# Optimization experiments

Hardware: AMD Instinct MI355X
Metric: run time of the kernel (lower is better)

The kernel has to match this reference:

```python
import jax, jax.numpy as jnp
import numpy as np

N_NODES = 10000
N_EDGES = 320000
IN_DIM = 256
HID = 64
HEADS = 4
OUT_DIM = 64
NEG_SLOPE = 0.2


def setup_inputs() -> dict:
    key = jax.random.key(0)
    ks = jax.random.split(key, 10)
    s = 0.05
    return {
        "h": jax.random.normal(ks[0], (N_NODES, IN_DIM), jnp.float32),
        "src": jax.random.randint(ks[1], (N_EDGES,), 0, N_NODES, jnp.int32),
        "dst": jax.random.randint(ks[2], (N_EDGES,), 0, N_NODES, jnp.int32),
        "W1": jax.random.normal(ks[3], (IN_DIM, HEADS * HID), jnp.float32) * s,
        "al1": jax.random.normal(ks[4], (HEADS, HID), jnp.float32) * s,
        "ar1": jax.random.normal(ks[5], (HEADS, HID), jnp.float32) * s,
        "b1": jnp.zeros((HEADS * HID,), jnp.float32),
        "W2": jax.random.normal(ks[6], (HEADS * HID, OUT_DIM), jnp.float32) * s,
        "al2": jax.random.normal(ks[7], (1, OUT_DIM), jnp.float32) * s,
        "ar2": jax.random.normal(ks[8], (1, OUT_DIM), jnp.float32) * s,
        "b2": jnp.zeros((OUT_DIM,), jnp.float32),
    }


def _gatconv(h, W, al, ar, b, src, dst, n_heads, d_out):
    """DGL-style GATConv: project, edge-softmax attention, scatter-aggregate."""
    n = h.shape[0]
    feat = (h @ W).reshape(n, n_heads, d_out)          # [N,H,D]
    el = jnp.sum(feat * al, axis=-1)                   # [N,H]
    er = jnp.sum(feat * ar, axis=-1)                   # [N,H]
    e = jax.nn.leaky_relu(el[src] + er[dst], NEG_SLOPE)  # [E,H]
    # segment softmax over incoming edges of each dst node
    m = jax.ops.segment_max(e, dst, num_segments=n)    # [N,H]
    ex = jnp.exp(e - m[dst])                           # [E,H]
    denom = jax.ops.segment_sum(ex, dst, num_segments=n)  # [N,H]
    alpha = ex / denom[dst]                            # [E,H]
    msg = feat[src] * alpha[:, :, None]                # [E,H,D]
    out = jax.ops.segment_sum(msg, dst, num_segments=n)  # [N,H,D]
    return out + b.reshape(n_heads, d_out)


def reference(h, src, dst, W1, al1, ar1, b1, W2, al2, ar2, b2):
    h1 = _gatconv(h, W1, al1, ar1, b1, src, dst, HEADS, HID)
    h1 = jax.nn.elu(h1.reshape(N_NODES, HEADS * HID))  # flatten(1) then ELU
    h2 = _gatconv(h1, W2, al2, ar2, b2, src, dst, 1, OUT_DIM)
    return jnp.squeeze(h2, axis=1)  # [N, OUT_DIM]
```

## Files before the change

### kernel.cpp

```cpp
#include <hip/hip_runtime.h>
#include <hip/hip_bf16.h>
#include <stdint.h>

#define NN 10000
#define NE 320000
#define NH 4
#define BCAP 128

#define GEMM1_MB 79
#define GEMM1_BLOCKS (GEMM1_MB * 4)
#define BUILD_BLOCKS 1250

typedef __attribute__((ext_vector_type(8))) short s16x8;
typedef __attribute__((ext_vector_type(4))) float f32x4;
typedef __attribute__((ext_vector_type(8))) unsigned short u16x8;

static __device__ __forceinline__ float b2f(unsigned short u) {
    union { unsigned int i; float f; } x; x.i = ((unsigned int)u) << 16; return x.f;
}
static __device__ __forceinline__ unsigned short f2b(float f) {
    unsigned int u = __float_as_uint(f);
    unsigned int r = (u + 0x7fffu + ((u >> 16) & 1u)) >> 16;
    return (unsigned short)r;
}

__global__ __launch_bounds__(256) void k_prep(const unsigned short* __restrict__ hraw,
                        const void* __restrict__ W1, const void* __restrict__ W2,
                        const void* al1, const void* ar1, const void* b1,
                        const void* al2, const void* ar2, const void* b2,
                        unsigned short* __restrict__ W1T, unsigned short* __restrict__ W2T,
                        unsigned short* __restrict__ canon, int* __restrict__ cnt,
                        int* __restrict__ flag) {
    __shared__ int sb[256];
    int t = threadIdx.x;
    int c = 0;
    for (int i = t; i < 2048; i += 256) {
        unsigned short u = hraw[i];
        int e = (u >> 7) & 0xFF;
        c += (e >= 97 && e <= 157) ? 1 : 0;
    }
    sb[t] = c;
    __syncthreads();
    for (int o = 128; o > 0; o >>= 1) {
        if (t < o) sb[t] += sb[t + o];
        __syncthreads();
    }
    int isbf = (sb[0] >= 1741) ? 1 : 0;

    int idx = blockIdx.x * 256 + t;
    if (idx < 65536) {
        int n = idx >> 8, k = idx & 255;
        W1T[idx] = isbf ? ((const unsigned short*)W1)[k * 256 + n]
                        : f2b(((const float*)W1)[k * 256 + n]);
    } else if (idx < 81920) {
        int j = idx - 65536;
        int n = j >> 8, k = j & 255;
        W2T[j] = isbf ? ((const unsigned short*)W2)[k * 64 + n]
                      : f2b(((const float*)W2)[k * 64 + n]);
    } else if (idx < 82880) {
        int j = idx - 81920;
        const void* srcp; int q;
        if      (j < 256) { srcp = al1; q = j; }
        else if (j < 512) { srcp = ar1; q = j - 256; }
        else if (j < 768) { srcp = b1;  q = j - 512; }
        else if (j < 832) { srcp = al2; q = j - 768; }
        else if (j < 896) { srcp = ar2; q = j - 832; }
        else              { srcp = b2;  q = j - 896; }
        canon[j] = isbf ? ((const unsigned short*)srcp)[q] : f2b(((const float*)srcp)[q]);
    } else if (idx < 92880) {
        cnt[idx - 82880] = 0;
    } else if (idx == 92880) {
        flag[0] = isbf;
    }
}

#define BSTRIDE 264
static __device__ __forceinline__ void gemm_body(short* Bs,
                        const void* __restrict__ A, const unsigned short* __restrict__ BT,
                        unsigned short* __restrict__ C,
                        float* __restrict__ el, float* __restrict__ er,
                        const unsigned short* __restrict__ al,
                        const unsigned short* __restrict__ ar,
                        int M, int N, int H, int a_isbf, int mtile, int head) {
    int t = threadIdx.x;
    int wave = t >> 6, lane = t & 63;
    int m0 = mtile * 128;
    const unsigned short* Bh = BT + (size_t)head * 64 * 256;

#pragma unroll
    for (int i = 0; i < 8; ++i) {
        int idx = t + i * 256;
        int row = idx >> 5, chunk = idx & 31;
        *(s16x8*)&Bs[row * BSTRIDE + chunk * 8] =
            *(const s16x8*)&Bh[(size_t)row * 256 + chunk * 8];
    }
    __syncthreads();

    int kq = (lane >> 4) * 8;
    const unsigned short* Ab = (const unsigned short*)A;
    const float*          Af = (const float*)A;
    int aR[2];
#pragma unroll
    for (int mi = 0; mi < 2; ++mi) {
        int aRow = m0 + mi * 64 + wave * 16 + (lane & 15);
        aR[mi] = (aRow < M) ? aRow : M - 1;
    }
    f32x4 acc[2][4] = {};

#pragma unroll
    for (int k0 = 0; k0 < 256; k0 += 32) {
        s16x8 afr[2];
#pragma unroll
        for (int mi = 0; mi < 2; ++mi) {
            if (a_isbf) {
                afr[mi] = *(const s16x8*)&Ab[(size_t)aR[mi] * 256 + k0 + kq];
            } else {
                const float* pf = &Af[(size_t)aR[mi] * 256 + k0 + kq];
                float4 x0 = *(const float4*)pf;
                float4 x1 = *(const float4*)(pf + 4);
                afr[mi][0] = (short)f2b(x0.x); afr[mi][1] = (short)f2b(x0.y);
                afr[mi][2] = (short)f2b(x0.z); afr[mi][3] = (short)f2b(x0.w);
                afr[mi][4] = (short)f2b(x1.x); afr[mi][5] = (short)f2b(x1.y);
                afr[mi][6] = (short)f2b(x1.z); afr[mi][7] = (short)f2b(x1.w);
            }
        }
#pragma unroll
        for (int nt = 0; nt < 4; ++nt) {
            s16x8 bfr = *(const s16x8*)&Bs[(nt * 16 + (lane & 15)) * BSTRIDE + k0 + kq];
            acc[0][nt] = __builtin_amdgcn_mfma_f32_16x16x32_bf16(afr[0], bfr, acc[0][nt], 0, 0, 0);
            acc[1][nt] = __builtin_amdgcn_mfma_f32_16x16x32_bf16(afr[1], bfr, acc[1][nt], 0, 0, 0);
        }
    }

    float alv[4], arv[4];
#pragma unroll
    for (int nt = 0; nt < 4; ++nt) {
        int c = (lane & 15) + nt * 16;
        alv[nt] = b2f(al[head * 64 + c]);
        arv[nt] = b2f(ar[head * 64 + c]);
    }
    int col0 = head * 64 + (lane & 15);
#pragma unroll
    for (int mi = 0; mi < 2; ++mi) {
        int r0 = m0 + mi * 64 + wave * 16 + (lane >> 4) * 4;
        float cr[4][4];
#pragma unroll
        for (int nt = 0; nt < 4; ++nt) {
            int col = col0 + nt * 16;
#pragma unroll
            for (int i = 0; i < 4; ++i) {
                unsigned short cb = f2b(acc[mi][nt][i]);
                cr[nt][i] = b2f(cb);
                int r = r0 + i;
                if (r < M) C[(size_t)r * N + col] = cb;
            }
        }
#pragma unroll
        for (int i = 0; i < 4; ++i) {
            float pl = 0.f, pr = 0.f;
#pragma unroll
            for (int nt = 0; nt < 4; ++nt) {
                pl += cr[nt][i] * alv[nt];
                pr += cr[nt][i] * arv[nt];
            }
#pragma unroll
            for (int o = 1; o < 16; o <<= 1) {
                pl += __shfl_xor(pl, o, 64);
                pr += __shfl_xor(pr, o, 64);
            }
            int r = r0 + i;
            if ((lane & 15) == 0 && r < M) {
                el[(size_t)r * H + head] = pl;
                er[(size_t)r * H + head] = pr;
            }
        }
    }
}

__global__ __launch_bounds__(256) void k_g1b(const void* __restrict__ A,
                        const unsigned short* __restrict__ W1T,
                        unsigned short* __restrict__ feat1,
                        float* __restrict__ el, float* __restrict__ er,
                        const unsigned short* __restrict__ al,
                        const unsigned short* __restrict__ ar,
                        const int* __restrict__ flagp,
                        const int* __restrict__ src, const int* __restrict__ dst,
                        int* __restrict__ cnt, int* __restrict__ bucket) {
    __shared__ short Bs[64 * BSTRIDE];
    int bid = blockIdx.x;
    if (bid < GEMM1_BLOCKS) {
        int head = bid / GEMM1_MB;
        int mtile = bid - head * GEMM1_MB;
        gemm_body(Bs, A, W1T, feat1, el, er, al, ar, NN, 256, NH, flagp[0], mtile, head);
    } else {
        int i = (bid - GEMM1_BLOCKS) * 256 + threadIdx.x;
        if (i < NE) {
            int d = dst[i];
            int pos = atomicAdd(&cnt[d], 1);
            if (pos < BCAP) bucket[(d << 7) + pos] = src[i];
        }
    }
}

__global__ __launch_bounds__(256) void k_gemm(const void* __restrict__ A,
                                              const unsigned short* __restrict__ BT,
                                              unsigned short* __restrict__ C,
                                              float* __restrict__ el, float* __restrict__ er,
                                              const unsigned short* __restrict__ al,
                                              const unsigned short* __restrict__ ar,
                                              int M, int N, int H) {
    __shared__ short Bs[64 * BSTRIDE];
    gemm_body(Bs, A, BT, C, el, er, al, ar, M, N, H, 1, blockIdx.x, blockIdx.y);
}

__global__ __launch_bounds__(256) void k_edge1(const int* __restrict__ cnt,
                        const int* __restrict__ bucket,
                        const float* __restrict__ el, const float* __restrict__ er,
                        const unsigned short* __restrict__ feat,
                        const unsigned short* __restrict__ b1,
                        unsigned short* __restrict__ h1) {
    __shared__ int   s_s[128];
    __shared__ float s_w[128][4];
    int node = blockIdx.x;
    int t = threadIdx.x;
    int head = t >> 6, lane = t & 63;
    int eg = lane >> 3, d8 = lane & 7;
    int end = cnt[node]; if (end > BCAP) end = BCAP;
    const int* bkt = bucket + ((size_t)node << 7);
    float4 er4 = *(const float4*)&er[(size_t)node * 4];
    float lsum = 0.f;
    float a[8] = {};
    for (int cbase = 0; cbase < end; cbase += 128) {
        int cn = end - cbase; if (cn > 128) cn = 128;
        __syncthreads();
        if (t < cn) {
            int s = bkt[cbase + t];
            s_s[t] = s;
            float4 el4 = *(const float4*)&el[(size_t)s * 4];
            float x0 = el4.x + er4.x; x0 = (x0 >= 0.f) ? x0 : 0.2f * x0;
            float x1 = el4.y + er4.y; x1 = (x1 >= 0.f) ? x1 : 0.2f * x1;
            float x2 = el4.z + er4.z; x2 = (x2 >= 0.f) ? x2 : 0.2f * x2;
            float x3 = el4.w + er4.w; x3 = (x3 >= 0.f) ? x3 : 0.2f * x3;
            s_w[t][0] = __expf(x0);
            s_w[t][1] = __expf(x1);
            s_w[t][2] = __expf(x2);
            s_w[t][3] = __expf(x3);
        } else if (t < ((cn + 7) & ~7)) {
            s_s[t] = 0;
            s_w[t][0] = 0.f; s_w[t][1] = 0.f; s_w[t][2] = 0.f; s_w[t][3] = 0.f;
        }
        __syncthreads();
        int niter = (cn + 7) >> 3;
#pragma unroll 2
        for (int i = 0; i < niter; ++i) {
            int idx = 8 * i + eg;
            float we = s_w[idx][head];
            int   se = s_s[idx];
            if (d8 == 0) lsum += we;
            u16x8 fv = *(const u16x8*)&feat[(((size_t)se * NH + head) << 6) + (d8 << 3)];
#pragma unroll
            for (int j = 0; j < 8; ++j) a[j] += we * b2f(fv[j]);
        }
    }
#pragma unroll
    for (int o = 1; o < 64; o <<= 1) lsum += __shfl_xor(lsum, o, 64);
#pragma unroll
    for (int j = 0; j < 8; ++j) {
        a[j] += __shfl_xor(a[j], 8, 64);
        a[j] += __shfl_xor(a[j], 16, 64);
        a[j] += __shfl_xor(a[j], 32, 64);
    }
    if (eg == 0) {
        float inv = (lsum > 0.f) ? 1.f / lsum : 0.f;
        u16x8 r;
#pragma unroll
        for (int j = 0; j < 8; ++j) {
            float o = a[j] * inv + b2f(b1[head * 64 + d8 * 8 + j]);
            o = (o > 0.f) ? o : (__expf(o) - 1.f);
            r[j] = f2b(o);
        }
        *(u16x8*)&h1[(((size_t)node * NH + head) << 6) + d8 * 8] = r;
    }
}

__global__ __launch_bounds__(256) void k_edge2(const int* __restrict__ cnt,
                        const int* __restrict__ bucket,
                        const float* __restrict__ el, const float* __restrict__ er,
                        const unsigned short* __restrict__ feat,
                        const unsigned short* __restrict__ b2,
                        void* __restrict__ out, const int* __restrict__ flagp) {
    int wave = threadIdx.x >> 6, lane = threadIdx.x & 63;
    int node = blockIdx.x * 4 + wave;
    if (node >= NN) return;
    int eg = lane >> 3, d8 = lane & 7;
    int isbf = flagp[0];
    int end = cnt[node]; if (end > BCAP) end = BCAP;
    const int* bkt = bucket + ((size_t)node << 7);
    float er_d = er[node];
    float lsum = 0.f;
    float a[8] = {};
    for (int base = 0; base < end; base += 64) {
        int c = base + lane;
        float wgt = 0.f; int s = 0;
        if (c < end) {
            s = bkt[c];
            float x = el[s] + er_d;
            x = (x >= 0.f) ? x : 0.2f * x;
            wgt = __expf(x);
        }
        lsum += wgt;
        int cn = end - base; if (cn > 64) cn = 64;
        int niter = (cn + 7) >> 3;
#pragma unroll 2
        for (int i = 0; i < niter; ++i) {
            int idx = 8 * i + eg;
            float we = __shfl(wgt, idx, 64);
            int   se = __shfl(s, idx, 64);
            u16x8 fv = *(const u16x8*)&feat[((size_t)se << 6) + (d8 << 3)];
#pragma unroll
            for (int j = 0; j < 8; ++j) a[j] += we * b2f(fv[j]);
        }
    }
#pragma unroll
    for (int o = 1; o < 64; o <<= 1) lsum += __shfl_xor(lsum, o, 64);
#pragma unroll
    for (int j = 0; j < 8; ++j) {
        a[j] += __shfl_xor(a[j], 8, 64);
        a[j] += __shfl_xor(a[j], 16, 64);
        a[j] += __shfl_xor(a[j], 32, 64);
    }
    if (eg == 0) {
        float inv = (lsum > 0.f) ? 1.f / lsum : 0.f;
        float o[8];
#pragma unroll
        for (int j = 0; j < 8; ++j) o[j] = a[j] * inv + b2f(b2[d8 * 8 + j]);
        size_t ob = ((size_t)node << 6) + d8 * 8;
        if (isbf) {
            u16x8 r;
#pragma unroll
            for (int j = 0; j < 8; ++j) r[j] = f2b(o[j]);
            *(u16x8*)&((unsigned short*)out)[ob] = r;
        } else {
            float4 r0, r1;
            r0.x = o[0]; r0.y = o[1]; r0.z = o[2]; r0.w = o[3];
            r1.x = o[4]; r1.y = o[5]; r1.z = o[6]; r1.w = o[7];
            *(float4*)&((float*)out)[ob] = r0;
            *(float4*)&((float*)out)[ob + 4] = r1;
        }
    }
}

extern "C" void kernel_launch(void* const* d_in, const int* in_sizes, int n_in,
                              void* d_out, int out_size, void* d_ws, size_t ws_size,
                              hipStream_t stream) {
    const void* h   = d_in[0];
    const int*  src = (const int*)d_in[1];
    const int*  dst = (const int*)d_in[2];
    const void* W1  = d_in[3];
    const void* al1 = d_in[4];
    const void* ar1 = d_in[5];
    const void* b1  = d_in[6];
    const void* W2  = d_in[7];
    const void* al2 = d_in[8];
    const void* ar2 = d_in[9];
    const void* b2  = d_in[10];

    char* w = (char*)d_ws;
    size_t off = 0;
    auto alloc = [&](size_t bytes) -> void* {
        void* p = w + off;
        off = (off + bytes + 255) & ~(size_t)255;
        return p;
    };
    int* flag               = (int*)alloc(8);
    int* cnt                = (int*)alloc(NN * 4);
    int* bucket             = (int*)alloc((size_t)NN * BCAP * 4);
    unsigned short* canon   = (unsigned short*)alloc(960 * 2);
    unsigned short* W1T     = (unsigned short*)alloc(256 * 256 * 2);
    unsigned short* W2T     = (unsigned short*)alloc(64 * 256 * 2);
    unsigned short* feat1   = (unsigned short*)alloc((size_t)NN * 256 * 2);
    float* el1              = (float*)alloc(NN * NH * 4);
    float* er1              = (float*)alloc(NN * NH * 4);
    unsigned short* h1      = (unsigned short*)alloc((size_t)NN * 256 * 2);
    unsigned short* feat2   = (unsigned short*)alloc((size_t)NN * 64 * 2);
    float* el2              = (float*)alloc(NN * 4);
    float* er2              = (float*)alloc(NN * 4);
    (void)ws_size; (void)in_sizes; (void)n_in; (void)out_size;

    unsigned short* cal1 = canon + 0;
    unsigned short* car1 = canon + 256;
    unsigned short* cb1  = canon + 512;
    unsigned short* cal2 = canon + 768;
    unsigned short* car2 = canon + 832;
    unsigned short* cb2  = canon + 896;

    k_prep<<<363, 256, 0, stream>>>((const unsigned short*)h, W1, W2,
                                    al1, ar1, b1, al2, ar2, b2,
                                    W1T, W2T, canon, cnt, flag);
    k_g1b<<<GEMM1_BLOCKS + BUILD_BLOCKS, 256, 0, stream>>>(h, W1T, feat1, el1, er1,
                                                           cal1, car1, flag,
                                                           src, dst, cnt, bucket);
    k_edge1<<<NN, 256, 0, stream>>>(cnt, bucket, el1, er1, feat1, cb1, h1);
    k_gemm<<<dim3(GEMM1_MB, 1), 256, 0, stream>>>(h1, W2T, feat2, el2, er2,
                                                  cal2, car2, NN, 64, 1);
    k_edge2<<<(NN + 3) / 4, 256, 0, stream>>>(cnt, bucket, el2, er2, feat2, cb2, d_out, flag);
}
```

Baseline: 153.6 us.

## Fuse layer-2 projection GEMM into layer-1 edge aggregation kernel

The layer-2 feature projection (h1 @ W2) and the el2/er2 attention logits are now computed per node inside the layer-1 aggregation kernel. Each block keeps its node's h1 row in shared memory and does a scalar 256x64 dot product, so the h1 buffer and the separate MFMA GEMM launch are no longer needed. In exchange, W2 is read by every block (from cache) and the MFMA GEMM becomes scalar FMAs, which adds work to an already heavy per-node kernel.

```diff
diff --git a/kernel.cpp b/kernel.cpp
--- a/kernel.cpp
+++ b/kernel.cpp
@@ -202,25 +202,20 @@
     }
 }
 
-__global__ __launch_bounds__(256) void k_gemm(const void* __restrict__ A,
-                                              const unsigned short* __restrict__ BT,
-                                              unsigned short* __restrict__ C,
-                                              float* __restrict__ el, float* __restrict__ er,
-                                              const unsigned short* __restrict__ al,
-                                              const unsigned short* __restrict__ ar,
-                                              int M, int N, int H) {
-    __shared__ short Bs[64 * BSTRIDE];
-    gemm_body(Bs, A, BT, C, el, er, al, ar, M, N, H, 1, blockIdx.x, blockIdx.y);
-}
-
 __global__ __launch_bounds__(256) void k_edge1(const int* __restrict__ cnt,
                         const int* __restrict__ bucket,
                         const float* __restrict__ el, const float* __restrict__ er,
                         const unsigned short* __restrict__ feat,
                         const unsigned short* __restrict__ b1,
-                        unsigned short* __restrict__ h1) {
+                        const unsigned short* __restrict__ W2T,
+                        const unsigned short* __restrict__ al2,
+                        const unsigned short* __restrict__ ar2,
+                        unsigned short* __restrict__ feat2,
+                        float* __restrict__ el2, float* __restrict__ er2) {
     __shared__ int   s_s[128];
     __shared__ float s_w[128][4];
+    __shared__ float h1s[256];
+    __shared__ float red[256];
     int node = blockIdx.x;
     int t = threadIdx.x;
     int head = t >> 6, lane = t & 63;
@@ -272,14 +267,40 @@
     }
     if (eg == 0) {
         float inv = (lsum > 0.f) ? 1.f / lsum : 0.f;
-        u16x8 r;
 #pragma unroll
         for (int j = 0; j < 8; ++j) {
             float o = a[j] * inv + b2f(b1[head * 64 + d8 * 8 + j]);
             o = (o > 0.f) ? o : (__expf(o) - 1.f);
-            r[j] = f2b(o);
-        }
-        *(u16x8*)&h1[(((size_t)node * NH + head) << 6) + d8 * 8] = r;
+            h1s[head * 64 + d8 * 8 + j] = b2f(f2b(o));
+        }
+    }
+    __syncthreads();
+    {
+        int n = t & 63, q = t >> 6;
+        const unsigned short* wp = &W2T[(size_t)n * 256 + q * 64];
+        float acc = 0.f;
+#pragma unroll
+        for (int k0 = 0; k0 < 64; k0 += 8) {
+            u16x8 wv = *(const u16x8*)&wp[k0];
+#pragma unroll
+            for (int j = 0; j < 8; ++j) acc += h1s[q * 64 + k0 + j] * b2f(wv[j]);
+        }
+        red[t] = acc;
+    }
+    __syncthreads();
+    if (t < 64) {
+        float fr = red[t] + red[64 + t] + red[128 + t] + red[192 + t];
+        unsigned short cb = f2b(fr);
+        feat2[((size_t)node << 6) + t] = cb;
+        float fv = b2f(cb);
+        float pl = fv * b2f(al2[t]);
+        float pr = fv * b2f(ar2[t]);
+#pragma unroll
+        for (int o = 1; o < 64; o <<= 1) {
+            pl += __shfl_xor(pl, o, 64);
+            pr += __shfl_xor(pr, o, 64);
+        }
+        if (t == 0) { el2[node] = pl; er2[node] = pr; }
     }
 }
 
@@ -381,7 +402,6 @@
     unsigned short* feat1   = (unsigned short*)alloc((size_t)NN * 256 * 2);
     float* el1              = (float*)alloc(NN * NH * 4);
     float* er1              = (float*)alloc(NN * NH * 4);
-    unsigned short* h1      = (unsigned short*)alloc((size_t)NN * 256 * 2);
     unsigned short* feat2   = (unsigned short*)alloc((size_t)NN * 64 * 2);
     float* el2              = (float*)alloc(NN * 4);
     float* er2              = (float*)alloc(NN * 4);
@@ -400,8 +420,7 @@
     k_g1b<<<GEMM1_BLOCKS + BUILD_BLOCKS, 256, 0, stream>>>(h, W1T, feat1, el1, er1,
                                                            cal1, car1, flag,
                                                            src, dst, cnt, bucket);
-    k_edge1<<<NN, 256, 0, stream>>>(cnt, bucket, el1, er1, feat1, cb1, h1);
-    k_gemm<<<dim3(GEMM1_MB, 1), 256, 0, stream>>>(h1, W2T, feat2, el2, er2,
-                                                  cal2, car2, NN, 64, 1);
+    k_edge1<<<NN, 256, 0, stream>>>(cnt, bucket, el1, er1, feat1, cb1,
+                                    W2T, cal2, car2, feat2, el2, er2);
     k_edge2<<<(NN + 3) / 4, 256, 0, stream>>>(cnt, bucket, el2, er2, feat2, cb2, d_out, flag);
 }
```

Result: slower. 184.7 us (+20.2%).

## Map one wave per node in layer-1 edge aggregation with shuffle-broadcast weights

Applied to the files above, without the earlier changes.

The layer-1 aggregation kernel moves from one 256-thread block per node (one wave per head, sharing weights through LDS with block barriers) to one wave per node handling all four heads in turn. Edge indices and attention weights are computed once per lane and broadcast with wave shuffles, so the shared memory and __syncthreads are gone. A fast path covers nodes with at most 64 incoming edges, and a chunked path with per-head accumulators covers larger degrees. This cuts barrier and launch-granularity overhead, but each wave now does four times the gather work serially and the general path holds more registers.

```diff
diff --git a/kernel.cpp b/kernel.cpp
--- a/kernel.cpp
+++ b/kernel.cpp
@@ -219,67 +219,117 @@
                         const unsigned short* __restrict__ feat,
                         const unsigned short* __restrict__ b1,
                         unsigned short* __restrict__ h1) {
-    __shared__ int   s_s[128];
-    __shared__ float s_w[128][4];
-    int node = blockIdx.x;
-    int t = threadIdx.x;
-    int head = t >> 6, lane = t & 63;
+    int wave = threadIdx.x >> 6, lane = threadIdx.x & 63;
+    int node = blockIdx.x * 4 + wave;
+    if (node >= NN) return;
     int eg = lane >> 3, d8 = lane & 7;
     int end = cnt[node]; if (end > BCAP) end = BCAP;
     const int* bkt = bucket + ((size_t)node << 7);
     float4 er4 = *(const float4*)&er[(size_t)node * 4];
-    float lsum = 0.f;
-    float a[8] = {};
-    for (int cbase = 0; cbase < end; cbase += 128) {
-        int cn = end - cbase; if (cn > 128) cn = 128;
-        __syncthreads();
-        if (t < cn) {
-            int s = bkt[cbase + t];
-            s_s[t] = s;
+
+    if (end <= 64) {
+        int s = 0;
+        float w0 = 0.f, w1 = 0.f, w2 = 0.f, w3 = 0.f;
+        if (lane < end) {
+            s = bkt[lane];
             float4 el4 = *(const float4*)&el[(size_t)s * 4];
             float x0 = el4.x + er4.x; x0 = (x0 >= 0.f) ? x0 : 0.2f * x0;
             float x1 = el4.y + er4.y; x1 = (x1 >= 0.f) ? x1 : 0.2f * x1;
             float x2 = el4.z + er4.z; x2 = (x2 >= 0.f) ? x2 : 0.2f * x2;
             float x3 = el4.w + er4.w; x3 = (x3 >= 0.f) ? x3 : 0.2f * x3;
-            s_w[t][0] = __expf(x0);
-            s_w[t][1] = __expf(x1);
-            s_w[t][2] = __expf(x2);
-            s_w[t][3] = __expf(x3);
-        } else if (t < ((cn + 7) & ~7)) {
-            s_s[t] = 0;
-            s_w[t][0] = 0.f; s_w[t][1] = 0.f; s_w[t][2] = 0.f; s_w[t][3] = 0.f;
-        }
-        __syncthreads();
-        int niter = (cn + 7) >> 3;
-#pragma unroll 2
-        for (int i = 0; i < niter; ++i) {
-            int idx = 8 * i + eg;
-            float we = s_w[idx][head];
-            int   se = s_s[idx];
-            if (d8 == 0) lsum += we;
-            u16x8 fv = *(const u16x8*)&feat[(((size_t)se * NH + head) << 6) + (d8 << 3)];
-#pragma unroll
-            for (int j = 0; j < 8; ++j) a[j] += we * b2f(fv[j]);
-        }
-    }
-#pragma unroll
-    for (int o = 1; o < 64; o <<= 1) lsum += __shfl_xor(lsum, o, 64);
-#pragma unroll
-    for (int j = 0; j < 8; ++j) {
-        a[j] += __shfl_xor(a[j], 8, 64);
-        a[j] += __shfl_xor(a[j], 16, 64);
-        a[j] += __shfl_xor(a[j], 32, 64);
-    }
-    if (eg == 0) {
-        float inv = (lsum > 0.f) ? 1.f / lsum : 0.f;
-        u16x8 r;
-#pragma unroll
-        for (int j = 0; j < 8; ++j) {
-            float o = a[j] * inv + b2f(b1[head * 64 + d8 * 8 + j]);
-            o = (o > 0.f) ? o : (__expf(o) - 1.f);
-            r[j] = f2b(o);
-        }
-        *(u16x8*)&h1[(((size_t)node * NH + head) << 6) + d8 * 8] = r;
+            w0 = __expf(x0); w1 = __expf(x1);
+            w2 = __expf(x2); w3 = __expf(x3);
+        }
+        int niter = (end + 7) >> 3;
+#pragma unroll
+        for (int h = 0; h < 4; ++h) {
+            float wh = (h == 0) ? w0 : (h == 1) ? w1 : (h == 2) ? w2 : w3;
+            float a[8] = {};
+            for (int i = 0; i < niter; ++i) {
+                int idx = 8 * i + eg;
+                float we = __shfl(wh, idx, 64);
+                int   se = __shfl(s, idx, 64);
+                u16x8 fv = *(const u16x8*)&feat[(((size_t)se * NH + h) << 6) + (d8 << 3)];
+#pragma unroll
+                for (int j = 0; j < 8; ++j) a[j] += we * b2f(fv[j]);
+            }
+            float ls = wh;
+#pragma unroll
+            for (int o = 1; o < 64; o <<= 1) ls += __shfl_xor(ls, o, 64);
+#pragma unroll
+            for (int j = 0; j < 8; ++j) {
+                a[j] += __shfl_xor(a[j], 8, 64);
+                a[j] += __shfl_xor(a[j], 16, 64);
+                a[j] += __shfl_xor(a[j], 32, 64);
+            }
+            if (eg == 0) {
+                float inv = (ls > 0.f) ? 1.f / ls : 0.f;
+                u16x8 r;
+#pragma unroll
+                for (int j = 0; j < 8; ++j) {
+                    float o = a[j] * inv + b2f(b1[h * 64 + d8 * 8 + j]);
+                    o = (o > 0.f) ? o : (__expf(o) - 1.f);
+                    r[j] = f2b(o);
+                }
+                *(u16x8*)&h1[(((size_t)node * NH + h) << 6) + d8 * 8] = r;
+            }
+        }
+    } else {
+        float a[4][8] = {};
+        float ls0 = 0.f, ls1 = 0.f, ls2 = 0.f, ls3 = 0.f;
+        for (int base = 0; base < end; base += 64) {
+            int c = base + lane;
+            int s = 0;
+            float w0 = 0.f, w1 = 0.f, w2 = 0.f, w3 = 0.f;
+            if (c < end) {
+                s = bkt[c];
+                float4 el4 = *(const float4*)&el[(size_t)s * 4];
+                float x0 = el4.x + er4.x; x0 = (x0 >= 0.f) ? x0 : 0.2f * x0;
+                float x1 = el4.y + er4.y; x1 = (x1 >= 0.f) ? x1 : 0.2f * x1;
+                float x2 = el4.z + er4.z; x2 = (x2 >= 0.f) ? x2 : 0.2f * x2;
+                float x3 = el4.w + er4.w; x3 = (x3 >= 0.f) ? x3 : 0.2f * x3;
+                w0 = __expf(x0); w1 = __expf(x1);
+                w2 = __expf(x2); w3 = __expf(x3);
+            }
+            ls0 += w0; ls1 += w1; ls2 += w2; ls3 += w3;
+            int cn = end - base; if (cn > 64) cn = 64;
+            int niter = (cn + 7) >> 3;
+#pragma unroll
+            for (int h = 0; h < 4; ++h) {
+                float wh = (h == 0) ? w0 : (h == 1) ? w1 : (h == 2) ? w2 : w3;
+                for (int i = 0; i < niter; ++i) {
+                    int idx = 8 * i + eg;
+                    float we = __shfl(wh, idx, 64);
+                    int   se = __shfl(s, idx, 64);
+                    u16x8 fv = *(const u16x8*)&feat[(((size_t)se * NH + h) << 6) + (d8 << 3)];
+#pragma unroll
+                    for (int j = 0; j < 8; ++j) a[h][j] += we * b2f(fv[j]);
+                }
+            }
+        }
+#pragma unroll
+        for (int h = 0; h < 4; ++h) {
+            float ls = (h == 0) ? ls0 : (h == 1) ? ls1 : (h == 2) ? ls2 : ls3;
+#pragma unroll
+            for (int o = 1; o < 64; o <<= 1) ls += __shfl_xor(ls, o, 64);
+#pragma unroll
+            for (int j = 0; j < 8; ++j) {
+                a[h][j] += __shfl_xor(a[h][j], 8, 64);
+                a[h][j] += __shfl_xor(a[h][j], 16, 64);
+                a[h][j] += __shfl_xor(a[h][j], 32, 64);
+            }
+            if (eg == 0) {
+                float inv = (ls > 0.f) ? 1.f / ls : 0.f;
+                u16x8 r;
+#pragma unroll
+                for (int j = 0; j < 8; ++j) {
+                    float o = a[h][j] * inv + b2f(b1[h * 64 + d8 * 8 + j]);
+                    o = (o > 0.f) ? o : (__expf(o) - 1.f);
+                    r[j] = f2b(o);
+                }
+                *(u16x8*)&h1[(((size_t)node * NH + h) << 6) + d8 * 8] = r;
+            }
+        }
     }
 }
 
@@ -400,7 +450,7 @@
     k_g1b<<<GEMM1_BLOCKS + BUILD_BLOCKS, 256, 0, stream>>>(h, W1T, feat1, el1, er1,
                                                            cal1, car1, flag,
                                                            src, dst, cnt, bucket);
-    k_edge1<<<NN, 256, 0, stream>>>(cnt, bucket, el1, er1, feat1, cb1, h1);
+    k_edge1<<<(NN + 3) / 4, 256, 0, stream>>>(cnt, bucket, el1, er1, feat1, cb1, h1);
     k_gemm<<<dim3(GEMM1_MB, 1), 256, 0, stream>>>(h1, W2T, feat2, el2, er2,
                                                   cal2, car2, NN, 64, 1);
     k_edge2<<<(NN + 3) / 4, 256, 0, stream>>>(cnt, bucket, el2, er2, feat2, cb2, d_out, flag);
```

Result: slower. 157.9 us (+2.8%).
